# Performance work log

Measured on AMD Instinct MI355X. Metric: run time of the kernel, lower is better.

The kernel has to match this reference:

```python
import jax, jax.numpy as jnp
import numpy as np

BATCH, N, FIN, FOUT = 131072, 16, 32, 32
NEG = -9.0e15


def setup_inputs() -> dict:
    key = jax.random.key(0)
    ks = jax.random.split(key, 8)
    stdv = 1.0 / np.sqrt(FOUT)
    return {
        "x": jax.random.normal(ks[0], (BATCH, N, FIN), dtype=jnp.float32),
        "basis": jax.random.normal(ks[1], (N, N), dtype=jnp.float32) * 0.25,
        "adj": jax.random.uniform(ks[2], (N, N), dtype=jnp.float32),  # all > 0 -> dense mask
        "e": jax.random.uniform(ks[3], (N, N), dtype=jnp.float32),    # edge weights at mask positions
        "W_e": jax.random.normal(ks[4], (FOUT * 10, FIN * 10), dtype=jnp.float32) * 0.02,
        "W_2": jax.random.normal(ks[5], (FOUT * 3, FIN * 3), dtype=jnp.float32) * 0.05,
        "W_3": jax.random.normal(ks[6], (FOUT * 3, FIN * 3), dtype=jnp.float32) * 0.05,
        "bias": jax.random.uniform(ks[7], (FOUT,), dtype=jnp.float32, minval=-stdv, maxval=stdv),
    }


def reference(x, basis, adj, e, W_e, W_2, W_3, bias):
    # x: [B, n, Fin]; basis: [n, n]
    Bsz = x.shape[0]
    # input.permute(2,0,1) @ B, then permute(1,0,2) -> [B, Fin, n]
    x_irrep = jnp.einsum('bnf,nm->bfm', x, basis)
    # three basis-block linears (torch F.linear: y = x @ W.T)
    out_e = (x_irrep[:, :, :10].reshape(Bsz, -1) @ W_e.T).reshape(Bsz, FOUT, 10)
    out_2 = (x_irrep[:, :, 10:13].reshape(Bsz, -1) @ W_2.T).reshape(Bsz, FOUT, 3)
    out_3 = (x_irrep[:, :, 13:].reshape(Bsz, -1) @ W_3.T).reshape(Bsz, FOUT, 3)
    out_irrep = jnp.concatenate([out_e, out_2, out_3], axis=2)  # [B, Fout, n]
    # (out_irrep @ B.T) then permute(0,2,1) -> [B, n, Fout]
    h = jnp.einsum('bon,mn->bmo', out_irrep, basis)
    # masked softmax adjacency; output = (softmax(adj) * I) @ h == diag-scale of h
    logits = jnp.where(adj > 0, e, NEG)
    adj_sm = jax.nn.softmax(logits, axis=1)
    diag = jnp.diagonal(adj_sm)  # [n]
    return h * diag[None, :, None] + bias[None, None, :]
```

## Files before the change

### kernel.cpp

```cpp
#include <hip/hip_runtime.h>
#include <hip/hip_bf16.h>

typedef __attribute__((ext_vector_type(4))) float f32x4_t;
typedef __attribute__((ext_vector_type(8))) short bf16x8_t;

__device__ __forceinline__ short f2bfs(float x) {
    union { __hip_bfloat16 h; short s; } u;
    u.h = __float2bfloat16(x);
    return u.s;
}

__device__ __forceinline__ void gload_lds16(const float* g, float* l) {
    __builtin_amdgcn_global_load_lds(
        (const __attribute__((address_space(1))) void*)g,
        (__attribute__((address_space(3))) void*)l, 16, 0, 0);
}

__global__ void build_M_kernel(const float* __restrict__ basis,
                               const float* __restrict__ adj,
                               const float* __restrict__ e,
                               const float* __restrict__ We,
                               const float* __restrict__ W2,
                               const float* __restrict__ W3,
                               unsigned short* __restrict__ Mfrag) {
    const int t = blockIdx.x * blockDim.x + threadIdx.x;
    const int c = t >> 9;
    const int k = t & 511;
    const int m  = c >> 5, o = c & 31;
    const int n2 = k >> 5, f = k & 31;

    float lv[16];
    float mx = -3.4e38f;
#pragma unroll
    for (int j = 0; j < 16; ++j) {
        float a = adj[m * 16 + j];
        float v = (a > 0.0f) ? e[m * 16 + j] : -9.0e15f;
        lv[j] = v;
        mx = fmaxf(mx, v);
    }
    float s = 0.0f;
#pragma unroll
    for (int j = 0; j < 16; ++j) s += expf(lv[j] - mx);
    const float dg = expf(lv[m] - mx) / s;

    float acc = 0.0f;
#pragma unroll
    for (int n = 0; n < 10; ++n) {
        float t2 = 0.0f;
#pragma unroll
        for (int m2 = 0; m2 < 10; ++m2)
            t2 += We[(o * 10 + n) * 320 + f * 10 + m2] * basis[n2 * 16 + m2];
        acc += basis[m * 16 + n] * t2;
    }
#pragma unroll
    for (int n = 0; n < 3; ++n) {
        float t2 = 0.0f;
#pragma unroll
        for (int m2 = 0; m2 < 3; ++m2)
            t2 += W2[(o * 3 + n) * 96 + f * 3 + m2] * basis[n2 * 16 + 10 + m2];
        acc += basis[m * 16 + 10 + n] * t2;
    }
#pragma unroll
    for (int n = 0; n < 3; ++n) {
        float t2 = 0.0f;
#pragma unroll
        for (int m2 = 0; m2 < 3; ++m2)
            t2 += W3[(o * 3 + n) * 96 + f * 3 + m2] * basis[n2 * 16 + 13 + m2];
        acc += basis[m * 16 + 13 + n] * t2;
    }

    const float Mv = dg * acc;

    const int ks = k >> 5;
    const int g  = (k >> 3) & 3;
    const int j  = k & 7;
    const int idx = ((ks * 32 + (c >> 4)) * 64 + ((c & 15) + 16 * g)) * 8 + j;
    Mfrag[idx] = (unsigned short)f2bfs(Mv);
}

__global__ __launch_bounds__(512, 4)
void gemm_kernel(const float* __restrict__ X,
                 const unsigned short* __restrict__ Mfrag,
                 const float* __restrict__ bias,
                 float* __restrict__ Y) {
    __shared__ float Atile[32 * 512];

    const int tid  = threadIdx.x;
    const int lane = tid & 63;
    const int wave = tid >> 6;
    const int l15  = lane & 15;
    const int g    = lane >> 4;
    const size_t rowbase = (size_t)blockIdx.x * 32;

    {
        const float* xb = X + rowbase * 512;
#pragma unroll
        for (int i = 0; i < 8; ++i) {
            const int row  = wave * 4 + (i >> 1);
            const int half = i & 1;
            float* ldst = &Atile[row * 512 + half * 256];
            const int lk4 = (half * 64 + lane) ^ (row & 7);
            gload_lds16(xb + row * 512 + lk4 * 4, ldst);
        }
    }
    __syncthreads();

    const int colbase = wave * 64;
    const unsigned short* bp = Mfrag + ((size_t)((colbase >> 4) * 64) + lane) * 8;
    const int s = l15 & 7;

    f32x4_t acc[2][4];
#pragma unroll
    for (int a = 0; a < 2; ++a)
#pragma unroll
        for (int b = 0; b < 4; ++b)
            acc[a][b] = (f32x4_t){0.f, 0.f, 0.f, 0.f};

#pragma unroll 4
    for (int ks = 0; ks < 16; ++ks) {
        bf16x8_t bfr[4];
#pragma unroll
        for (int ni = 0; ni < 4; ++ni)
            bfr[ni] = *reinterpret_cast<const bf16x8_t*>(bp + ks * 16384 + ni * 512);

        bf16x8_t a[2];
#pragma unroll
        for (int mi = 0; mi < 2; ++mi) {
            const int row = mi * 16 + l15;
            const int pl  = ks * 8 + ((g * 2) ^ s);
            const int ph  = ks * 8 + ((g * 2 + 1) ^ s);
            f32x4_t lo = *reinterpret_cast<const f32x4_t*>(&Atile[row * 512 + pl * 4]);
            f32x4_t hi = *reinterpret_cast<const f32x4_t*>(&Atile[row * 512 + ph * 4]);
#pragma unroll
            for (int j = 0; j < 4; ++j) {
                a[mi][j]     = f2bfs(lo[j]);
                a[mi][j + 4] = f2bfs(hi[j]);
            }
        }
#pragma unroll
        for (int mi = 0; mi < 2; ++mi)
#pragma unroll
            for (int ni = 0; ni < 4; ++ni)
                acc[mi][ni] = __builtin_amdgcn_mfma_f32_16x16x32_bf16(
                    a[mi], bfr[ni], acc[mi][ni], 0, 0, 0);
    }

    __syncthreads();

    float* scr = Atile + wave * 2048;
    const float b_lo = bias[l15];
    const float b_hi = bias[16 + l15];

#pragma unroll
    for (int mi = 0; mi < 2; ++mi)
#pragma unroll
        for (int ni = 0; ni < 4; ++ni) {
            const float bb = (ni & 1) ? b_hi : b_lo;
#pragma unroll
            for (int r = 0; r < 4; ++r)
                scr[(mi * 16 + g * 4 + r) * 64 + ni * 16 + l15] = acc[mi][ni][r] + bb;
        }

#pragma unroll
    for (int it = 0; it < 8; ++it) {
        const int flat = it * 64 + lane;
        const int row  = flat >> 4;
        const int c4   = flat & 15;
        f32x4_t v = *reinterpret_cast<const f32x4_t*>(&scr[row * 64 + c4 * 4]);
        float* yp = Y + (rowbase + row) * 512 + colbase + c4 * 4;
        __builtin_nontemporal_store(v, reinterpret_cast<f32x4_t*>(yp));
    }
}

extern "C" void kernel_launch(void* const* d_in, const int* in_sizes, int n_in,
                              void* d_out, int out_size, void* d_ws, size_t ws_size,
                              hipStream_t stream) {
    const float* x     = (const float*)d_in[0];
    const float* basis = (const float*)d_in[1];
    const float* adj   = (const float*)d_in[2];
    const float* e     = (const float*)d_in[3];
    const float* We    = (const float*)d_in[4];
    const float* W2    = (const float*)d_in[5];
    const float* W3    = (const float*)d_in[6];
    const float* bias  = (const float*)d_in[7];

    unsigned short* Mfrag = (unsigned short*)d_ws;
    if (ws_size < 512u * 512u * 2u) return;

    const int Bsz = in_sizes[0] / 512;
    build_M_kernel<<<512, 512, 0, stream>>>(basis, adj, e, We, W2, W3, Mfrag);
    gemm_kernel<<<Bsz / 32, 512, 0, stream>>>(x, Mfrag, bias, (float*)d_out);
}
```

Before: 140.8 us.

## Convert X to bf16 MFMA fragments on load to shrink LDS and double occupancy

```diff
diff --git a/kernel.cpp b/kernel.cpp
--- a/kernel.cpp
+++ b/kernel.cpp
@@ -8,12 +8,6 @@
     union { __hip_bfloat16 h; short s; } u;
     u.h = __float2bfloat16(x);
     return u.s;
-}
-
-__device__ __forceinline__ void gload_lds16(const float* g, float* l) {
-    __builtin_amdgcn_global_load_lds(
-        (const __attribute__((address_space(1))) void*)g,
-        (__attribute__((address_space(3))) void*)l, 16, 0, 0);
 }
 
 __global__ void build_M_kernel(const float* __restrict__ basis,
@@ -78,12 +72,13 @@
     Mfrag[idx] = (unsigned short)f2bfs(Mv);
 }
 
-__global__ __launch_bounds__(512, 4)
+__global__ __launch_bounds__(512, 8)
 void gemm_kernel(const float* __restrict__ X,
                  const unsigned short* __restrict__ Mfrag,
                  const float* __restrict__ bias,
                  float* __restrict__ Y) {
-    __shared__ float Atile[32 * 512];
+    __shared__ float lds_f32[8704];
+    unsigned short* Afrag = reinterpret_cast<unsigned short*>(lds_f32);
 
     const int tid  = threadIdx.x;
     const int lane = tid & 63;
@@ -95,19 +90,26 @@
     {
         const float* xb = X + rowbase * 512;
 #pragma unroll
-        for (int i = 0; i < 8; ++i) {
-            const int row  = wave * 4 + (i >> 1);
-            const int half = i & 1;
-            float* ldst = &Atile[row * 512 + half * 256];
-            const int lk4 = (half * 64 + lane) ^ (row & 7);
-            gload_lds16(xb + row * 512 + lk4 * 4, ldst);
+        for (int i = 0; i < 4; ++i) {
+            const int f   = wave * 4 + i;
+            const int row = (f & 1) * 16 + l15;
+            const int k0  = (f >> 1) * 32 + g * 8;
+            const float* src = xb + (size_t)row * 512 + k0;
+            f32x4_t v0 = *reinterpret_cast<const f32x4_t*>(src);
+            f32x4_t v1 = *reinterpret_cast<const f32x4_t*>(src + 4);
+            bf16x8_t bv;
+#pragma unroll
+            for (int j = 0; j < 4; ++j) {
+                bv[j]     = f2bfs(v0[j]);
+                bv[j + 4] = f2bfs(v1[j]);
+            }
+            *reinterpret_cast<bf16x8_t*>(&Afrag[((f * 64) + lane) * 8]) = bv;
         }
     }
     __syncthreads();
 
     const int colbase = wave * 64;
     const unsigned short* bp = Mfrag + ((size_t)((colbase >> 4) * 64) + lane) * 8;
-    const int s = l15 & 7;
 
     f32x4_t acc[2][4];
 #pragma unroll
@@ -116,27 +118,16 @@
         for (int b = 0; b < 4; ++b)
             acc[a][b] = (f32x4_t){0.f, 0.f, 0.f, 0.f};
 
-#pragma unroll 4
+#pragma unroll
     for (int ks = 0; ks < 16; ++ks) {
         bf16x8_t bfr[4];
 #pragma unroll
         for (int ni = 0; ni < 4; ++ni)
-            bfr[ni] = *reinterpret_cast<const bf16x8_t*>(bp + ks * 16384 + ni * 512);
-
+            bfr[ni] = *reinterpret_cast<const bf16x8_t*>(bp + (size_t)ks * 16384 + ni * 512);
         bf16x8_t a[2];
 #pragma unroll
-        for (int mi = 0; mi < 2; ++mi) {
-            const int row = mi * 16 + l15;
-            const int pl  = ks * 8 + ((g * 2) ^ s);
-            const int ph  = ks * 8 + ((g * 2 + 1) ^ s);
-            f32x4_t lo = *reinterpret_cast<const f32x4_t*>(&Atile[row * 512 + pl * 4]);
-            f32x4_t hi = *reinterpret_cast<const f32x4_t*>(&Atile[row * 512 + ph * 4]);
-#pragma unroll
-            for (int j = 0; j < 4; ++j) {
-                a[mi][j]     = f2bfs(lo[j]);
-                a[mi][j + 4] = f2bfs(hi[j]);
-            }
-        }
+        for (int mi = 0; mi < 2; ++mi)
+            a[mi] = *reinterpret_cast<const bf16x8_t*>(&Afrag[((ks * 2 + mi) * 64 + lane) * 8]);
 #pragma unroll
         for (int mi = 0; mi < 2; ++mi)
 #pragma unroll
@@ -147,28 +138,29 @@
 
     __syncthreads();
 
-    float* scr = Atile + wave * 2048;
+    constexpr int SW = 68;
+    float* scr = lds_f32 + wave * (16 * SW);
     const float b_lo = bias[l15];
     const float b_hi = bias[16 + l15];
 
 #pragma unroll
-    for (int mi = 0; mi < 2; ++mi)
+    for (int mi = 0; mi < 2; ++mi) {
 #pragma unroll
         for (int ni = 0; ni < 4; ++ni) {
             const float bb = (ni & 1) ? b_hi : b_lo;
 #pragma unroll
             for (int r = 0; r < 4; ++r)
-                scr[(mi * 16 + g * 4 + r) * 64 + ni * 16 + l15] = acc[mi][ni][r] + bb;
+                scr[(g * 4 + r) * SW + ni * 16 + l15] = acc[mi][ni][r] + bb;
         }
-
 #pragma unroll
-    for (int it = 0; it < 8; ++it) {
-        const int flat = it * 64 + lane;
-        const int row  = flat >> 4;
-        const int c4   = flat & 15;
-        f32x4_t v = *reinterpret_cast<const f32x4_t*>(&scr[row * 64 + c4 * 4]);
-        float* yp = Y + (rowbase + row) * 512 + colbase + c4 * 4;
-        __builtin_nontemporal_store(v, reinterpret_cast<f32x4_t*>(yp));
+        for (int it = 0; it < 4; ++it) {
+            const int flat = it * 64 + lane;
+            const int row  = flat >> 4;
+            const int c4   = flat & 15;
+            f32x4_t v = *reinterpret_cast<const f32x4_t*>(&scr[row * SW + c4 * 4]);
+            float* yp = Y + (rowbase + mi * 16 + row) * 512 + colbase + c4 * 4;
+            __builtin_nontemporal_store(v, reinterpret_cast<f32x4_t*>(yp));
+        }
     }
 }
 
```

After: 215.4 us. +52.9%, slower.
